# Optimization experiments

Measured on AMD Instinct MI355X. Metric: run time of the kernel, lower is better.

## Reference

```python
import jax, jax.numpy as jnp
import numpy as np

N_NODES = 100000
N_EDGES = 1600000
IN_DIM = 128
HIDDEN = 128
EPS = 1e-5  # BatchNorm1d default eps


def gcn_conv(x, src, dst, W, b, n_nodes):
    """PyG GCNConv with default add_self_loops=True, edge_weight=None.
    out = D^{-1/2} (A + I) D^{-1/2} X W + b, deg computed from dst (col)."""
    xw = x @ W  # [N, out_dim] -- transform before propagate, as in PyG
    ones = jnp.ones((src.shape[0],), dtype=x.dtype)
    deg = jax.ops.segment_sum(ones, dst, num_segments=n_nodes) + 1.0  # +1 self-loop
    dis = jax.lax.rsqrt(deg)  # deg >= 1 always
    norm = dis[src] * dis[dst]  # [E]
    msgs = xw[src] * norm[:, None]  # [E, out_dim] gather (irregular access)
    agg = jax.ops.segment_sum(msgs, dst, num_segments=n_nodes)
    agg = agg + xw * (1.0 / deg)[:, None]  # self-loop contribution, norm = 1/deg_i
    return agg + b


def batch_norm(x, gamma, beta):
    # training-mode BatchNorm1d: biased batch statistics over the node dim
    m = jnp.mean(x, axis=0)
    v = jnp.mean(jnp.square(x - m), axis=0)
    return gamma * (x - m) * jax.lax.rsqrt(v + EPS) + beta


def setup_inputs() -> dict:
    key = jax.random.key(0)
    ks = jax.random.split(key, 6)
    x = jax.random.normal(ks[0], (N_NODES, IN_DIM), dtype=jnp.float32)
    edge_index = jax.random.randint(ks[1], (2, N_EDGES), 0, N_NODES, dtype=jnp.int64)
    # Glorot-ish scaled weights
    W1 = jax.random.normal(ks[2], (IN_DIM, HIDDEN), dtype=jnp.float32) / np.sqrt(IN_DIM)
    W2 = jax.random.normal(ks[3], (HIDDEN, HIDDEN // 2), dtype=jnp.float32) / np.sqrt(HIDDEN)
    Wf = jax.random.normal(ks[4], (HIDDEN // 2, 1), dtype=jnp.float32) / np.sqrt(HIDDEN // 2)
    return {
        "x": x,
        "edge_index": edge_index,
        "W1": W1, "b1": jnp.zeros((HIDDEN,), jnp.float32),
        "g1": jnp.ones((HIDDEN,), jnp.float32), "beta1": jnp.zeros((HIDDEN,), jnp.float32),
        "W2": W2, "b2": jnp.zeros((HIDDEN // 2,), jnp.float32),
        "g2": jnp.ones((HIDDEN // 2,), jnp.float32), "beta2": jnp.zeros((HIDDEN // 2,), jnp.float32),
        "Wf": Wf, "bf": jnp.zeros((1,), jnp.float32),
    }


def reference(x, edge_index, W1, b1, g1, beta1, W2, b2, g2, beta2, Wf, bf):
    src, dst = edge_index[0], edge_index[1]
    n = x.shape[0]
    h = jax.nn.relu(batch_norm(gcn_conv(x, src, dst, W1, b1, n), g1, beta1))
    # dropout is identity in eval / correctness-baseline mode
    h = jax.nn.relu(batch_norm(gcn_conv(h, src, dst, W2, b2, n), g2, beta2))
    return h @ Wf + bf  # [N, 1]
```

## Files before the change

### kernel.cpp

```cpp
#include <hip/hip_runtime.h>

#define NN 100000
#define NE 1600000
#define D1 128
#define D2 64
#define BN_EPS 1e-5f
#define SCAN_CHUNK 512
#define NB_SCAN ((NN + SCAN_CHUNK - 1) / SCAN_CHUNK)

typedef unsigned int uint32;
typedef unsigned long long u64;
typedef unsigned short ushort;
typedef __attribute__((ext_vector_type(8))) short bf16x8;
typedef __attribute__((ext_vector_type(4))) float f32x4;

__device__ __forceinline__ ushort f2bf1(float f) {
    uint32 u = __float_as_uint(f);
    return (ushort)((u + 0x7FFFu + ((u >> 16) & 1u)) >> 16);
}
__device__ __forceinline__ float bf_lo(uint32 v) { return __uint_as_float(v << 16); }
__device__ __forceinline__ float bf_hi(uint32 v) { return __uint_as_float(v & 0xFFFF0000u); }

__global__ __launch_bounds__(256) void cnt_k(const int* __restrict__ dst,
                                             int* __restrict__ cnt) {
    int i = blockIdx.x * 256 + threadIdx.x;
    if (i < NE) atomicAdd(&cnt[dst[i]], 1);
}

__global__ __launch_bounds__(256) void make_dis_k(const int* __restrict__ cnt,
                                                  float* __restrict__ dis) {
    int i = blockIdx.x * 256 + threadIdx.x;
    if (i < NN) dis[i] = rsqrtf((float)cnt[i] + 1.0f);
}

__global__ __launch_bounds__(SCAN_CHUNK) void scan1_k(const int* __restrict__ cnt,
                                                      int* __restrict__ rowptr,
                                                      int* __restrict__ bsum) {
    __shared__ int sh[SCAN_CHUNK];
    int tid = threadIdx.x;
    int g = blockIdx.x * SCAN_CHUNK + tid;
    int v = (g < NN) ? cnt[g] : 0;
    sh[tid] = v;
    __syncthreads();
    for (int o = 1; o < SCAN_CHUNK; o <<= 1) {
        int t = (tid >= o) ? sh[tid - o] : 0;
        __syncthreads();
        sh[tid] += t;
        __syncthreads();
    }
    if (g < NN) rowptr[g] = sh[tid] - v;
    if (tid == SCAN_CHUNK - 1) bsum[blockIdx.x] = sh[tid];
}

__global__ void scan2_k(int* __restrict__ bsum) {
    if (threadIdx.x == 0 && blockIdx.x == 0) {
        int a = 0;
        for (int i = 0; i < NB_SCAN; ++i) { int t = bsum[i]; bsum[i] = a; a += t; }
    }
}

__global__ __launch_bounds__(256) void scan3_k(int* __restrict__ rowptr,
                                               const int* __restrict__ bsum) {
    int g = blockIdx.x * 256 + threadIdx.x;
    if (g < NN) rowptr[g] += bsum[g >> 9];
    if (g == 0) rowptr[NN] = NE;
}

__global__ __launch_bounds__(256) void fill_k(const int* __restrict__ src,
                                              const int* __restrict__ dst,
                                              const int* __restrict__ rowptr,
                                              const float* __restrict__ dis,
                                              int* __restrict__ cur,
                                              u64* __restrict__ edges) {
    int e = blockIdx.x * 256 + threadIdx.x;
    if (e >= NE) return;
    int d = dst[e];
    int s = src[e];
    int p = rowptr[d] + atomicAdd(&cur[d], 1);
    u64 pk = ((u64)__float_as_uint(dis[s] * dis[d]) << 32) | (uint32)s;
    edges[p] = pk;
}

__global__ void bncoef_k(const float* __restrict__ sums, const float* __restrict__ ssq,
                         const float* __restrict__ g, const float* __restrict__ beta,
                         float* __restrict__ coef, int dim) {
    int c = threadIdx.x;
    if (c >= dim) return;
    float m = sums[c] * (1.0f / NN);
    float var = ssq[c] * (1.0f / NN) - m * m;
    float sc = g[c] * rsqrtf(var + BN_EPS);
    coef[c] = sc;
    coef[dim + c] = beta[c] - m * sc;
}

__global__ __launch_bounds__(256) void wt_k(const float* __restrict__ W1,
                                            const float* __restrict__ W2,
                                            ushort* __restrict__ wt1,
                                            ushort* __restrict__ wt2) {
    int i = blockIdx.x * 256 + threadIdx.x;
    if (i < 128 * 128) {
        int c = i >> 7, k = i & 127;
        wt1[i] = f2bf1(W1[k * 128 + c]);
    } else if (i < 128 * 128 + 64 * 128) {
        int o = i - 128 * 128;
        int c = o >> 7, k = o & 127;
        wt2[o] = f2bf1(W2[k * 64 + c]);
    }
}

template<int OUT, bool FUSE_BN>
__global__ __launch_bounds__(256) void mgemm_k(const float* __restrict__ X,
                                               const ushort* __restrict__ Wt,
                                               const float* __restrict__ coef,
                                               ushort* __restrict__ Yb) {
    const int lane = threadIdx.x & 63;
    const int wv = threadIdx.x >> 6;
    const int row0 = blockIdx.x * 64 + wv * 16;
    const int m = lane & 15;
    const int kg = lane >> 4;
    const int rowA = min(row0 + m, NN - 1);
    f32x4 acc[OUT / 16];
    #pragma unroll
    for (int t = 0; t < OUT / 16; ++t) acc[t] = (f32x4){0.f, 0.f, 0.f, 0.f};

    #pragma unroll
    for (int kc = 0; kc < 128; kc += 32) {
        const int k0 = kc + kg * 8;
        float4 xa = *(const float4*)(X + (size_t)rowA * 128 + k0);
        float4 xb = *(const float4*)(X + (size_t)rowA * 128 + k0 + 4);
        if constexpr (FUSE_BN) {
            float4 sa = *(const float4*)(coef + k0);
            float4 sb = *(const float4*)(coef + k0 + 4);
            float4 ha = *(const float4*)(coef + 128 + k0);
            float4 hb = *(const float4*)(coef + 128 + k0 + 4);
            xa.x = fmaxf(fmaf(xa.x, sa.x, ha.x), 0.f);
            xa.y = fmaxf(fmaf(xa.y, sa.y, ha.y), 0.f);
            xa.z = fmaxf(fmaf(xa.z, sa.z, ha.z), 0.f);
            xa.w = fmaxf(fmaf(xa.w, sa.w, ha.w), 0.f);
            xb.x = fmaxf(fmaf(xb.x, sb.x, hb.x), 0.f);
            xb.y = fmaxf(fmaf(xb.y, sb.y, hb.y), 0.f);
            xb.z = fmaxf(fmaf(xb.z, sb.z, hb.z), 0.f);
            xb.w = fmaxf(fmaf(xb.w, sb.w, hb.w), 0.f);
        }
        bf16x8 af;
        af[0] = (short)f2bf1(xa.x); af[1] = (short)f2bf1(xa.y);
        af[2] = (short)f2bf1(xa.z); af[3] = (short)f2bf1(xa.w);
        af[4] = (short)f2bf1(xb.x); af[5] = (short)f2bf1(xb.y);
        af[6] = (short)f2bf1(xb.z); af[7] = (short)f2bf1(xb.w);
        #pragma unroll
        for (int t = 0; t < OUT / 16; ++t) {
            bf16x8 bf = *(const bf16x8*)(Wt + (size_t)(t * 16 + m) * 128 + k0);
            acc[t] = __builtin_amdgcn_mfma_f32_16x16x32_bf16(af, bf, acc[t], 0, 0, 0);
        }
    }
    #pragma unroll
    for (int t = 0; t < OUT / 16; ++t) {
        #pragma unroll
        for (int r = 0; r < 4; ++r) {
            int rr = row0 + kg * 4 + r;
            if (rr < NN) Yb[(size_t)rr * OUT + t * 16 + m] = f2bf1(acc[t][r]);
        }
    }
}

__global__ __launch_bounds__(256) void agg128_k(const int* __restrict__ rowptr,
                                                const u64* __restrict__ edges,
                                                const float* __restrict__ dis,
                                                const uint32* __restrict__ xwb,
                                                const float* __restrict__ b,
                                                float* __restrict__ agg,
                                                float* __restrict__ sums,
                                                float* __restrict__ ssq) {
    const int lane = threadIdx.x & 63;
    const int wid = (blockIdx.x * 256 + threadIdx.x) >> 6;
    const int nwaves = gridDim.x * 4;
    float s0 = 0.f, s1 = 0.f, q0 = 0.f, q1 = 0.f;
    const float bc0 = b[lane * 2], bc1 = b[lane * 2 + 1];

    for (int n = wid; n < NN; n += nwaves) {
        const int beg = rowptr[n], end = rowptr[n + 1];
        const float dn = dis[n];
        float ax = 0.f, ay = 0.f;
        int e = beg;
        for (; e + 8 <= end; e += 8) {
            u64 ed[8]; uint32 vv[8]; float ww[8];
            #pragma unroll
            for (int j = 0; j < 8; ++j) ed[j] = edges[e + j];
            #pragma unroll
            for (int j = 0; j < 8; ++j) {
                vv[j] = xwb[(size_t)(uint32)ed[j] * 64 + lane];
                ww[j] = __uint_as_float((uint32)(ed[j] >> 32));
            }
            #pragma unroll
            for (int j = 0; j < 8; ++j) {
                ax = fmaf(bf_lo(vv[j]), ww[j], ax);
                ay = fmaf(bf_hi(vv[j]), ww[j], ay);
            }
        }
        for (; e < end; ++e) {
            u64 ed = edges[e];
            float w = __uint_as_float((uint32)(ed >> 32));
            uint32 v = xwb[(size_t)(uint32)ed * 64 + lane];
            ax = fmaf(bf_lo(v), w, ax);
            ay = fmaf(bf_hi(v), w, ay);
        }
        float sl = dn * dn;
        uint32 xv = xwb[(size_t)n * 64 + lane];
        ax = fmaf(bf_lo(xv), sl, ax) + bc0;
        ay = fmaf(bf_hi(xv), sl, ay) + bc1;
        u64 o = ((u64)__float_as_uint(ay) << 32) | __float_as_uint(ax);
        __builtin_nontemporal_store(o, (u64*)&agg[(size_t)n * 128 + lane * 2]);
        s0 += ax; q0 = fmaf(ax, ax, q0);
        s1 += ay; q1 = fmaf(ay, ay, q1);
    }

    __shared__ float ls[256];
    ls[threadIdx.x] = 0.f;
    __syncthreads();
    atomicAdd(&ls[lane * 2], s0);
    atomicAdd(&ls[lane * 2 + 1], s1);
    atomicAdd(&ls[128 + lane * 2], q0);
    atomicAdd(&ls[128 + lane * 2 + 1], q1);
    __syncthreads();
    if (threadIdx.x < 128) atomicAdd(&sums[threadIdx.x], ls[threadIdx.x]);
    else atomicAdd(&ssq[threadIdx.x - 128], ls[threadIdx.x]);
}

__global__ __launch_bounds__(256) void agg64_k(const int* __restrict__ rowptr,
                                               const u64* __restrict__ edges,
                                               const float* __restrict__ dis,
                                               const uint32* __restrict__ xwb,
                                               const float* __restrict__ b,
                                               float* __restrict__ agg,
                                               float* __restrict__ sums,
                                               float* __restrict__ ssq) {
    const int lane = threadIdx.x & 63;
    const int half = lane >> 5;
    const int sl = lane & 31;
    const int wid = (blockIdx.x * 256 + threadIdx.x) >> 6;
    const int nwaves = gridDim.x * 4;
    float s0 = 0.f, s1 = 0.f, q0 = 0.f, q1 = 0.f;
    const float bc0 = b[sl * 2], bc1 = b[sl * 2 + 1];

    for (int n = wid; n < NN; n += nwaves) {
        const int beg = rowptr[n], end = rowptr[n + 1];
        const float dn = dis[n];
        float ax = 0.f, ay = 0.f;
        int e = beg;
        for (; e + 16 <= end; e += 16) {
            u64 ed[8]; uint32 vv[8]; float ww[8];
            #pragma unroll
            for (int j = 0; j < 8; ++j) ed[j] = edges[e + 2 * j + half];
            #pragma unroll
            for (int j = 0; j < 8; ++j) {
                vv[j] = xwb[(size_t)(uint32)ed[j] * 32 + sl];
                ww[j] = __uint_as_float((uint32)(ed[j] >> 32));
            }
            #pragma unroll
            for (int j = 0; j < 8; ++j) {
                ax = fmaf(bf_lo(vv[j]), ww[j], ax);
                ay = fmaf(bf_hi(vv[j]), ww[j], ay);
            }
        }
        for (; e + 2 <= end; e += 2) {
            u64 ed = edges[e + half];
            float w = __uint_as_float((uint32)(ed >> 32));
            uint32 v = xwb[(size_t)(uint32)ed * 32 + sl];
            ax = fmaf(bf_lo(v), w, ax);
            ay = fmaf(bf_hi(v), w, ay);
        }
        if (e < end && half == 0) {
            u64 ed = edges[e];
            float w = __uint_as_float((uint32)(ed >> 32));
            uint32 v = xwb[(size_t)(uint32)ed * 32 + sl];
            ax = fmaf(bf_lo(v), w, ax);
            ay = fmaf(bf_hi(v), w, ay);
        }
        ax += __shfl_down(ax, 32);
        ay += __shfl_down(ay, 32);
        if (half == 0) {
            float slf = dn * dn;
            uint32 xv = xwb[(size_t)n * 32 + sl];
            ax = fmaf(bf_lo(xv), slf, ax) + bc0;
            ay = fmaf(bf_hi(xv), slf, ay) + bc1;
            u64 o = ((u64)__float_as_uint(ay) << 32) | __float_as_uint(ax);
            __builtin_nontemporal_store(o, (u64*)&agg[(size_t)n * 64 + sl * 2]);
            s0 += ax; q0 = fmaf(ax, ax, q0);
            s1 += ay; q1 = fmaf(ay, ay, q1);
        }
    }

    __shared__ float ls[128];
    if (threadIdx.x < 128) ls[threadIdx.x] = 0.f;
    __syncthreads();
    if (half == 0) {
        atomicAdd(&ls[sl * 2], s0);
        atomicAdd(&ls[sl * 2 + 1], s1);
        atomicAdd(&ls[64 + sl * 2], q0);
        atomicAdd(&ls[64 + sl * 2 + 1], q1);
    }
    __syncthreads();
    if (threadIdx.x < 64) atomicAdd(&sums[threadIdx.x], ls[threadIdx.x]);
    else if (threadIdx.x < 128) atomicAdd(&ssq[threadIdx.x - 64], ls[threadIdx.x]);
}

__global__ __launch_bounds__(256) void final_k(const float* __restrict__ h,
                                               const float* __restrict__ coef,
                                               const float* __restrict__ Wf,
                                               const float* __restrict__ bf,
                                               float* __restrict__ out) {
    int wid = (blockIdx.x * 256 + threadIdx.x) >> 6;
    int lane = threadIdx.x & 63;
    if (wid >= NN) return;
    float v = fmaxf(fmaf(h[(size_t)wid * 64 + lane], coef[lane], coef[64 + lane]), 0.f)
              * Wf[lane];
    #pragma unroll
    for (int o = 32; o > 0; o >>= 1) v += __shfl_down(v, o);
    if (lane == 0) out[wid] = v + bf[0];
}

extern "C" void kernel_launch(void* const* d_in, const int* in_sizes, int n_in,
                              void* d_out, int out_size, void* d_ws, size_t ws_size,
                              hipStream_t stream) {
    const float* x   = (const float*)d_in[0];
    const int*   ei  = (const int*)d_in[1];
    const int*   src = ei;
    const int*   dst = ei + NE;
    const float* W1  = (const float*)d_in[2];
    const float* b1  = (const float*)d_in[3];
    const float* g1  = (const float*)d_in[4];
    const float* be1 = (const float*)d_in[5];
    const float* W2  = (const float*)d_in[6];
    const float* b2  = (const float*)d_in[7];
    const float* g2  = (const float*)d_in[8];
    const float* be2 = (const float*)d_in[9];
    const float* Wf  = (const float*)d_in[10];
    const float* bf  = (const float*)d_in[11];
    float* out = (float*)d_out;

    uint32* xwb  = (uint32*)d_ws;
    float* agg1  = (float*)(xwb + (size_t)NN * 64);
    float* agg2  = agg1  + (size_t)NN * D1;
    float* dis   = agg2  + (size_t)NN * D2;
    float* sums1 = dis   + NN;
    float* ssq1  = sums1 + D1;
    float* sums2 = ssq1  + D1;
    float* ssq2  = sums2 + D2;
    float* coef1 = ssq2  + D2;
    float* coef2 = coef1 + 2 * D1;
    ushort* wt1  = (ushort*)(coef2 + 2 * D2);
    ushort* wt2  = wt1 + 128 * 128;
    int*   cnt    = (int*)(wt2 + 64 * 128);
    int*   cur    = cnt + NN;
    int*   rowptr = cur + NN;
    int*   bsum   = rowptr + NN + 1;
    u64*   edges  = (u64*)(((size_t)(bsum + 256) + 7) & ~(size_t)7);

    hipMemsetAsync(cnt, 0, sizeof(int) * 2 * NN, stream);
    hipMemsetAsync(sums1, 0, sizeof(float) * (2 * D1 + 2 * D2), stream);

    cnt_k<<<(NE + 255) / 256, 256, 0, stream>>>(dst, cnt);
    make_dis_k<<<(NN + 255) / 256, 256, 0, stream>>>(cnt, dis);
    scan1_k<<<NB_SCAN, SCAN_CHUNK, 0, stream>>>(cnt, rowptr, bsum);
    scan2_k<<<1, 64, 0, stream>>>(bsum);
    scan3_k<<<(NN + 255) / 256, 256, 0, stream>>>(rowptr, bsum);
    fill_k<<<(NE + 255) / 256, 256, 0, stream>>>(src, dst, rowptr, dis, cur, edges);
    wt_k<<<(128 * 128 + 64 * 128 + 255) / 256, 256, 0, stream>>>(W1, W2, wt1, wt2);

    mgemm_k<128, false><<<(NN + 63) / 64, 256, 0, stream>>>(x, wt1, nullptr, (ushort*)xwb);
    agg128_k<<<4096, 256, 0, stream>>>(rowptr, edges, dis, xwb, b1, agg1, sums1, ssq1);
    bncoef_k<<<1, 128, 0, stream>>>(sums1, ssq1, g1, be1, coef1, D1);

    mgemm_k<64, true><<<(NN + 63) / 64, 256, 0, stream>>>(agg1, wt2, coef1, (ushort*)xwb);
    agg64_k<<<4096, 256, 0, stream>>>(rowptr, edges, dis, xwb, b2, agg2, sums2, ssq2);
    bncoef_k<<<1, 64, 0, stream>>>(sums2, ssq2, g2, be2, coef2, D2);

    final_k<<<(NN * 64 + 255) / 256, 256, 0, stream>>>(agg2, coef2, Wf, bf, out);
}
```

Baseline: 515.7 us.

## Store layer-1 aggregate in bf16, split edge arrays, halve aggregation grids

Layer-1 aggregation now writes its output as packed bf16 instead of fp32, and the second GEMM reads those bf16 values directly. This halves the write and read traffic of the 100k×128 intermediate. The packed 64-bit edge records become separate index and weight arrays, with loads grouped so all gathers are issued before the FMAs. Aggregation grids drop from 4096 to 2048 blocks and the agg64 store is no longer nontemporal. The cost is extra bf16 rounding before batch norm, and the change risks slightly lower accuracy.

```diff
diff --git a/kernel.cpp b/kernel.cpp
--- a/kernel.cpp
+++ b/kernel.cpp
@@ -17,6 +17,12 @@
 __device__ __forceinline__ ushort f2bf1(float f) {
     uint32 u = __float_as_uint(f);
     return (ushort)((u + 0x7FFFu + ((u >> 16) & 1u)) >> 16);
+}
+__device__ __forceinline__ uint32 f2bf_pair(float a, float b) {
+    uint32 ua = __float_as_uint(a), ub = __float_as_uint(b);
+    ua = (ua + 0x7FFFu + ((ua >> 16) & 1u)) >> 16;
+    ub = (ub + 0x7FFFu + ((ub >> 16) & 1u)) >> 16;
+    return ua | (ub << 16);
 }
 __device__ __forceinline__ float bf_lo(uint32 v) { return __uint_as_float(v << 16); }
 __device__ __forceinline__ float bf_hi(uint32 v) { return __uint_as_float(v & 0xFFFF0000u); }
@@ -71,14 +77,15 @@
                                               const int* __restrict__ rowptr,
                                               const float* __restrict__ dis,
                                               int* __restrict__ cur,
-                                              u64* __restrict__ edges) {
+                                              int* __restrict__ esrc,
+                                              float* __restrict__ ew) {
     int e = blockIdx.x * 256 + threadIdx.x;
     if (e >= NE) return;
     int d = dst[e];
     int s = src[e];
     int p = rowptr[d] + atomicAdd(&cur[d], 1);
-    u64 pk = ((u64)__float_as_uint(dis[s] * dis[d]) << 32) | (uint32)s;
-    edges[p] = pk;
+    esrc[p] = s;
+    ew[p] = dis[s] * dis[d];
 }
 
 __global__ void bncoef_k(const float* __restrict__ sums, const float* __restrict__ ssq,
@@ -108,8 +115,8 @@
     }
 }
 
-template<int OUT, bool FUSE_BN>
-__global__ __launch_bounds__(256) void mgemm_k(const float* __restrict__ X,
+template<int OUT, bool BF16BN>
+__global__ __launch_bounds__(256) void mgemm_k(const void* __restrict__ Xv,
                                                const ushort* __restrict__ Wt,
                                                const float* __restrict__ coef,
                                                ushort* __restrict__ Yb) {
@@ -126,31 +133,40 @@
     #pragma unroll
     for (int kc = 0; kc < 128; kc += 32) {
         const int k0 = kc + kg * 8;
-        float4 xa = *(const float4*)(X + (size_t)rowA * 128 + k0);
-        float4 xb = *(const float4*)(X + (size_t)rowA * 128 + k0 + 4);
-        if constexpr (FUSE_BN) {
+        float xs[8];
+        if constexpr (BF16BN) {
+            const ushort* Xb = (const ushort*)Xv;
+            uint4 raw = *(const uint4*)(Xb + (size_t)rowA * 128 + k0);
+            xs[0] = bf_lo(raw.x); xs[1] = bf_hi(raw.x);
+            xs[2] = bf_lo(raw.y); xs[3] = bf_hi(raw.y);
+            xs[4] = bf_lo(raw.z); xs[5] = bf_hi(raw.z);
+            xs[6] = bf_lo(raw.w); xs[7] = bf_hi(raw.w);
             float4 sa = *(const float4*)(coef + k0);
             float4 sb = *(const float4*)(coef + k0 + 4);
             float4 ha = *(const float4*)(coef + 128 + k0);
             float4 hb = *(const float4*)(coef + 128 + k0 + 4);
-            xa.x = fmaxf(fmaf(xa.x, sa.x, ha.x), 0.f);
-            xa.y = fmaxf(fmaf(xa.y, sa.y, ha.y), 0.f);
-            xa.z = fmaxf(fmaf(xa.z, sa.z, ha.z), 0.f);
-            xa.w = fmaxf(fmaf(xa.w, sa.w, ha.w), 0.f);
-            xb.x = fmaxf(fmaf(xb.x, sb.x, hb.x), 0.f);
-            xb.y = fmaxf(fmaf(xb.y, sb.y, hb.y), 0.f);
-            xb.z = fmaxf(fmaf(xb.z, sb.z, hb.z), 0.f);
-            xb.w = fmaxf(fmaf(xb.w, sb.w, hb.w), 0.f);
+            xs[0] = fmaxf(fmaf(xs[0], sa.x, ha.x), 0.f);
+            xs[1] = fmaxf(fmaf(xs[1], sa.y, ha.y), 0.f);
+            xs[2] = fmaxf(fmaf(xs[2], sa.z, ha.z), 0.f);
+            xs[3] = fmaxf(fmaf(xs[3], sa.w, ha.w), 0.f);
+            xs[4] = fmaxf(fmaf(xs[4], sb.x, hb.x), 0.f);
+            xs[5] = fmaxf(fmaf(xs[5], sb.y, hb.y), 0.f);
+            xs[6] = fmaxf(fmaf(xs[6], sb.z, hb.z), 0.f);
+            xs[7] = fmaxf(fmaf(xs[7], sb.w, hb.w), 0.f);
+        } else {
+            const float* X = (const float*)Xv;
+            float4 xa = *(const float4*)(X + (size_t)rowA * 128 + k0);
+            float4 xb = *(const float4*)(X + (size_t)rowA * 128 + k0 + 4);
+            xs[0] = xa.x; xs[1] = xa.y; xs[2] = xa.z; xs[3] = xa.w;
+            xs[4] = xb.x; xs[5] = xb.y; xs[6] = xb.z; xs[7] = xb.w;
         }
         bf16x8 af;
-        af[0] = (short)f2bf1(xa.x); af[1] = (short)f2bf1(xa.y);
-        af[2] = (short)f2bf1(xa.z); af[3] = (short)f2bf1(xa.w);
-        af[4] = (short)f2bf1(xb.x); af[5] = (short)f2bf1(xb.y);
-        af[6] = (short)f2bf1(xb.z); af[7] = (short)f2bf1(xb.w);
+        #pragma unroll
+        for (int i = 0; i < 8; ++i) af[i] = (short)f2bf1(xs[i]);
         #pragma unroll
         for (int t = 0; t < OUT / 16; ++t) {
-            bf16x8 bf = *(const bf16x8*)(Wt + (size_t)(t * 16 + m) * 128 + k0);
-            acc[t] = __builtin_amdgcn_mfma_f32_16x16x32_bf16(af, bf, acc[t], 0, 0, 0);
+            bf16x8 bfr = *(const bf16x8*)(Wt + (size_t)(t * 16 + m) * 128 + k0);
+            acc[t] = __builtin_amdgcn_mfma_f32_16x16x32_bf16(af, bfr, acc[t], 0, 0, 0);
         }
     }
     #pragma unroll
@@ -164,11 +180,12 @@
 }
 
 __global__ __launch_bounds__(256) void agg128_k(const int* __restrict__ rowptr,
-                                                const u64* __restrict__ edges,
+                                                const int* __restrict__ esrc,
+                                                const float* __restrict__ ew,
                                                 const float* __restrict__ dis,
                                                 const uint32* __restrict__ xwb,
                                                 const float* __restrict__ b,
-                                                float* __restrict__ agg,
+                                                uint32* __restrict__ agg1b,
                                                 float* __restrict__ sums,
                                                 float* __restrict__ ssq) {
     const int lane = threadIdx.x & 63;
@@ -183,24 +200,24 @@
         float ax = 0.f, ay = 0.f;
         int e = beg;
         for (; e + 8 <= end; e += 8) {
-            u64 ed[8]; uint32 vv[8]; float ww[8];
-            #pragma unroll
-            for (int j = 0; j < 8; ++j) ed[j] = edges[e + j];
+            int idx[8]; float w[8]; uint32 vv[8];
+            #pragma unroll
+            for (int j = 0; j < 8; ++j) idx[j] = esrc[e + j];
+            #pragma unroll
+            for (int j = 0; j < 8; ++j) w[j] = ew[e + j];
+            #pragma unroll
+            for (int j = 0; j < 8; ++j)
+                vv[j] = xwb[(size_t)idx[j] * 64 + lane];
             #pragma unroll
             for (int j = 0; j < 8; ++j) {
-                vv[j] = xwb[(size_t)(uint32)ed[j] * 64 + lane];
-                ww[j] = __uint_as_float((uint32)(ed[j] >> 32));
+                ax = fmaf(bf_lo(vv[j]), w[j], ax);
+                ay = fmaf(bf_hi(vv[j]), w[j], ay);
             }
-            #pragma unroll
-            for (int j = 0; j < 8; ++j) {
-                ax = fmaf(bf_lo(vv[j]), ww[j], ax);
-                ay = fmaf(bf_hi(vv[j]), ww[j], ay);
-            }
         }
         for (; e < end; ++e) {
-            u64 ed = edges[e];
-            float w = __uint_as_float((uint32)(ed >> 32));
-            uint32 v = xwb[(size_t)(uint32)ed * 64 + lane];
+            int s = esrc[e];
+            float w = ew[e];
+            uint32 v = xwb[(size_t)s * 64 + lane];
             ax = fmaf(bf_lo(v), w, ax);
             ay = fmaf(bf_hi(v), w, ay);
         }
@@ -208,8 +225,7 @@
         uint32 xv = xwb[(size_t)n * 64 + lane];
         ax = fmaf(bf_lo(xv), sl, ax) + bc0;
         ay = fmaf(bf_hi(xv), sl, ay) + bc1;
-        u64 o = ((u64)__float_as_uint(ay) << 32) | __float_as_uint(ax);
-        __builtin_nontemporal_store(o, (u64*)&agg[(size_t)n * 128 + lane * 2]);
+        agg1b[(size_t)n * 64 + lane] = f2bf_pair(ax, ay);
         s0 += ax; q0 = fmaf(ax, ax, q0);
         s1 += ay; q1 = fmaf(ay, ay, q1);
     }
@@ -227,7 +243,8 @@
 }
 
 __global__ __launch_bounds__(256) void agg64_k(const int* __restrict__ rowptr,
-                                               const u64* __restrict__ edges,
+                                               const int* __restrict__ esrc,
+                                               const float* __restrict__ ew,
                                                const float* __restrict__ dis,
                                                const uint32* __restrict__ xwb,
                                                const float* __restrict__ b,
@@ -248,31 +265,31 @@
         float ax = 0.f, ay = 0.f;
         int e = beg;
         for (; e + 16 <= end; e += 16) {
-            u64 ed[8]; uint32 vv[8]; float ww[8];
-            #pragma unroll
-            for (int j = 0; j < 8; ++j) ed[j] = edges[e + 2 * j + half];
+            int idx[8]; float w[8]; uint32 vv[8];
+            #pragma unroll
+            for (int j = 0; j < 8; ++j) idx[j] = esrc[e + 2 * j + half];
+            #pragma unroll
+            for (int j = 0; j < 8; ++j) w[j] = ew[e + 2 * j + half];
+            #pragma unroll
+            for (int j = 0; j < 8; ++j)
+                vv[j] = xwb[(size_t)idx[j] * 32 + sl];
             #pragma unroll
             for (int j = 0; j < 8; ++j) {
-                vv[j] = xwb[(size_t)(uint32)ed[j] * 32 + sl];
-                ww[j] = __uint_as_float((uint32)(ed[j] >> 32));
+                ax = fmaf(bf_lo(vv[j]), w[j], ax);
+                ay = fmaf(bf_hi(vv[j]), w[j], ay);
             }
-            #pragma unroll
-            for (int j = 0; j < 8; ++j) {
-                ax = fmaf(bf_lo(vv[j]), ww[j], ax);
-                ay = fmaf(bf_hi(vv[j]), ww[j], ay);
-            }
         }
         for (; e + 2 <= end; e += 2) {
-            u64 ed = edges[e + half];
-            float w = __uint_as_float((uint32)(ed >> 32));
-            uint32 v = xwb[(size_t)(uint32)ed * 32 + sl];
+            int s = esrc[e + half];
+            float w = ew[e + half];
+            uint32 v = xwb[(size_t)s * 32 + sl];
             ax = fmaf(bf_lo(v), w, ax);
             ay = fmaf(bf_hi(v), w, ay);
         }
         if (e < end && half == 0) {
-            u64 ed = edges[e];
-            float w = __uint_as_float((uint32)(ed >> 32));
-            uint32 v = xwb[(size_t)(uint32)ed * 32 + sl];
+            int s = esrc[e];
+            float w = ew[e];
+            uint32 v = xwb[(size_t)s * 32 + sl];
             ax = fmaf(bf_lo(v), w, ax);
             ay = fmaf(bf_hi(v), w, ay);
         }
@@ -283,8 +300,7 @@
             uint32 xv = xwb[(size_t)n * 32 + sl];
             ax = fmaf(bf_lo(xv), slf, ax) + bc0;
             ay = fmaf(bf_hi(xv), slf, ay) + bc1;
-            u64 o = ((u64)__float_as_uint(ay) << 32) | __float_as_uint(ax);
-            __builtin_nontemporal_store(o, (u64*)&agg[(size_t)n * 64 + sl * 2]);
+            *(float2*)&agg[(size_t)n * 64 + sl * 2] = make_float2(ax, ay);
             s0 += ax; q0 = fmaf(ax, ax, q0);
             s1 += ay; q1 = fmaf(ay, ay, q1);
         }
@@ -338,23 +354,24 @@
     const float* bf  = (const float*)d_in[11];
     float* out = (float*)d_out;
 
-    uint32* xwb  = (uint32*)d_ws;
-    float* agg1  = (float*)(xwb + (size_t)NN * 64);
-    float* agg2  = agg1  + (size_t)NN * D1;
-    float* dis   = agg2  + (size_t)NN * D2;
-    float* sums1 = dis   + NN;
-    float* ssq1  = sums1 + D1;
-    float* sums2 = ssq1  + D1;
-    float* ssq2  = sums2 + D2;
-    float* coef1 = ssq2  + D2;
-    float* coef2 = coef1 + 2 * D1;
-    ushort* wt1  = (ushort*)(coef2 + 2 * D2);
-    ushort* wt2  = wt1 + 128 * 128;
-    int*   cnt    = (int*)(wt2 + 64 * 128);
-    int*   cur    = cnt + NN;
-    int*   rowptr = cur + NN;
-    int*   bsum   = rowptr + NN + 1;
-    u64*   edges  = (u64*)(((size_t)(bsum + 256) + 7) & ~(size_t)7);
+    uint32* xwb   = (uint32*)d_ws;
+    uint32* agg1b = xwb + (size_t)NN * 64;
+    float*  agg2  = (float*)(agg1b + (size_t)NN * 64);
+    float*  dis   = agg2 + (size_t)NN * D2;
+    float*  sums1 = dis + NN;
+    float*  ssq1  = sums1 + D1;
+    float*  sums2 = ssq1 + D1;
+    float*  ssq2  = sums2 + D2;
+    float*  coef1 = ssq2 + D2;
+    float*  coef2 = coef1 + 2 * D1;
+    ushort* wt1   = (ushort*)(coef2 + 2 * D2);
+    ushort* wt2   = wt1 + 128 * 128;
+    int*    cnt    = (int*)(wt2 + 64 * 128);
+    int*    cur    = cnt + NN;
+    int*    rowptr = cur + NN;
+    int*    bsum   = rowptr + NN + 1;
+    int*    esrc   = bsum + 256;
+    float*  ew     = (float*)(esrc + NE);
 
     hipMemsetAsync(cnt, 0, sizeof(int) * 2 * NN, stream);
     hipMemsetAsync(sums1, 0, sizeof(float) * (2 * D1 + 2 * D2), stream);
@@ -364,15 +381,15 @@
     scan1_k<<<NB_SCAN, SCAN_CHUNK, 0, stream>>>(cnt, rowptr, bsum);
     scan2_k<<<1, 64, 0, stream>>>(bsum);
     scan3_k<<<(NN + 255) / 256, 256, 0, stream>>>(rowptr, bsum);
-    fill_k<<<(NE + 255) / 256, 256, 0, stream>>>(src, dst, rowptr, dis, cur, edges);
+    fill_k<<<(NE + 255) / 256, 256, 0, stream>>>(src, dst, rowptr, dis, cur, esrc, ew);
     wt_k<<<(128 * 128 + 64 * 128 + 255) / 256, 256, 0, stream>>>(W1, W2, wt1, wt2);
 
     mgemm_k<128, false><<<(NN + 63) / 64, 256, 0, stream>>>(x, wt1, nullptr, (ushort*)xwb);
-    agg128_k<<<4096, 256, 0, stream>>>(rowptr, edges, dis, xwb, b1, agg1, sums1, ssq1);
+    agg128_k<<<2048, 256, 0, stream>>>(rowptr, esrc, ew, dis, xwb, b1, agg1b, sums1, ssq1);
     bncoef_k<<<1, 128, 0, stream>>>(sums1, ssq1, g1, be1, coef1, D1);
 
-    mgemm_k<64, true><<<(NN + 63) / 64, 256, 0, stream>>>(agg1, wt2, coef1, (ushort*)xwb);
-    agg64_k<<<4096, 256, 0, stream>>>(rowptr, edges, dis, xwb, b2, agg2, sums2, ssq2);
+    mgemm_k<64, true><<<(NN + 63) / 64, 256, 0, stream>>>(agg1b, wt2, coef1, (ushort*)xwb);
+    agg64_k<<<2048, 256, 0, stream>>>(rowptr, esrc, ew, dis, xwb, b2, agg2, sums2, ssq2);
     bncoef_k<<<1, 64, 0, stream>>>(sums2, ssq2, g2, be2, coef2, D2);
 
     final_k<<<(NN * 64 + 255) / 256, 256, 0, stream>>>(agg2, coef2, Wf, bf, out);
```

Result: faster. 446.7 us (-13.4%).
